# Kernel optimization log

Hardware: AMD Instinct MI355X
Metric: run time of the kernel (lower is better)

Reference implementation:

```python
import jax, jax.numpy as jnp
import numpy as np

B, H, W, C = 16, 64, 64, 512
NH, HD = 16, 32
WH = WW = 8
SHIFT = 4
N = WH * WW
NWIN = (H // WH) * (W // WW)
EPS = 1e-6


def _rel_coords_table():
    rh = np.arange(-(WH - 1), WH, dtype=np.float32)
    rw = np.arange(-(WW - 1), WW, dtype=np.float32)
    t = np.expand_dims(np.transpose(np.stack(np.meshgrid(rh, rw)), (1, 2, 0)), 0)
    t[:, :, :, 0] /= WH - 1
    t[:, :, :, 1] /= WW - 1
    t *= 8
    t = np.sign(t) * np.log2(np.abs(t) + 1.0) / np.log2(8)
    return jnp.asarray(t, jnp.float32)  # (1, 2*WW-1, 2*WH-1, 2)


def _rel_pos_index():
    gx, gy = np.meshgrid(np.arange(WH), np.arange(WW))
    coords = np.stack([gy, gx]).reshape(2, -1)
    rel = (coords[:, :, None] - coords[:, None, :]).transpose(1, 2, 0)
    rel[:, :, 0] += WH - 1
    rel[:, :, 1] += WW - 1
    rel[:, :, 0] *= 2 * WW - 1
    return jnp.asarray(rel.sum(-1).reshape(-1), jnp.int32)  # (N*N,)


def _attn_mask():
    img = np.zeros((H, W), np.float32)
    cnt = 0
    for hs in (slice(0, -WH), slice(-WH, -SHIFT), slice(-SHIFT, None)):
        for ws in (slice(0, -WW), slice(-WW, -SHIFT), slice(-SHIFT, None)):
            img[hs, ws] = cnt
            cnt += 1
    mw = img.reshape(H // WH, WH, W // WW, WW).transpose(0, 2, 1, 3).reshape(-1, N)
    am = mw[:, None, :] - mw[:, :, None]
    return jnp.asarray(np.where(am == 0, 0.0, -100.0), jnp.float32)  # (nW, N, N)


REL_TABLE = _rel_coords_table()
REL_IDX = _rel_pos_index()
ATTN_MASK = _attn_mask()


def _ln(x, g, b):
    m = jnp.mean(x, -1, keepdims=True)
    v = jnp.var(x, -1, keepdims=True)
    return (x - m) * jax.lax.rsqrt(v + EPS) * g + b


def _forward(x, q_w, q_b, k_w, v_w, v_b, proj_w, proj_b, tau,
             cpb_w1, cpb_b1, cpb_w2, cpb_b2,
             norm1_g, norm1_b, norm2_g, norm2_b,
             mlp_w1, mlp_b1, mlp_w2, mlp_b2):
    shortcut = x
    xs = x.reshape(B, H, W, C)
    xs = jnp.roll(xs, shift=(-SHIFT, -SHIFT), axis=(1, 2))  # cyclic shift
    # window partition -> (B*nW, N, C)
    xw = xs.reshape(B, H // WH, WH, W // WW, WW, C).transpose(0, 1, 3, 2, 4, 5).reshape(-1, N, C)
    Bw = B * NWIN
    q = (xw @ q_w + q_b).reshape(Bw, N, NH, HD).transpose(0, 2, 1, 3)
    k = (xw @ k_w).reshape(Bw, N, NH, HD).transpose(0, 2, 1, 3)
    v = (xw @ v_w + v_b).reshape(Bw, N, NH, HD).transpose(0, 2, 1, 3)
    # cosine attention
    qn = jnp.linalg.norm(q, axis=-1)[..., :, None]
    kn = jnp.linalg.norm(k, axis=-1)[..., None, :]
    denom = jnp.maximum(qn * kn, 1e-6)
    attn = jnp.einsum('bhnd,bhmd->bhnm', q, k) / denom
    logit_scale = jnp.maximum(tau + jnp.log(10.0), 0.01)  # (1, NH, 1, 1)
    attn = attn * logit_scale
    # continuous relative position bias MLP
    tbl = jax.nn.relu(REL_TABLE @ cpb_w1 + cpb_b1) @ cpb_w2 + cpb_b2
    tbl = tbl.reshape(-1, NH)
    bias = tbl[REL_IDX].reshape(N, N, NH).transpose(2, 0, 1)
    bias = 16.0 * jax.nn.sigmoid(bias)
    attn = attn + bias[None]
    # shifted-window mask
    attn = attn.reshape(B, NWIN, NH, N, N) + ATTN_MASK[None, :, None]
    attn = jax.nn.softmax(attn.reshape(Bw, NH, N, N), axis=-1)
    out = jnp.einsum('bhnm,bhmd->bhnd', attn, v).transpose(0, 2, 1, 3).reshape(Bw, N, C)
    out = out @ proj_w + proj_b
    # window reverse + reverse shift
    out = out.reshape(B, H // WH, W // WW, WH, WW, C).transpose(0, 1, 3, 2, 4, 5).reshape(B, H, W, C)
    out = jnp.roll(out, shift=(SHIFT, SHIFT), axis=(1, 2)).reshape(B, H * W, C)
    # Swin-V2 post-norm residuals
    x = shortcut + _ln(out, norm1_g, norm1_b)
    h = jax.nn.gelu(x @ mlp_w1 + mlp_b1) @ mlp_w2 + mlp_b2
    x = x + _ln(h, norm2_g, norm2_b)
    return x


def setup_inputs() -> dict:
    key = jax.random.key(0)
    ks = jax.random.split(key, 10)
    s = 0.02
    return {
        'x': jax.random.normal(ks[0], (B, H * W, C), jnp.float32),
        'q_w': jax.random.normal(ks[1], (C, C), jnp.float32) * s,
        'q_b': jnp.zeros((C,), jnp.float32),
        'k_w': jax.random.normal(ks[2], (C, C), jnp.float32) * s,
        'v_w': jax.random.normal(ks[3], (C, C), jnp.float32) * s,
        'v_b': jnp.zeros((C,), jnp.float32),
        'proj_w': jax.random.normal(ks[4], (C, C), jnp.float32) * s,
        'proj_b': jnp.zeros((C,), jnp.float32),
        'tau': jax.random.normal(ks[5], (1, NH, 1, 1), jnp.float32) * s,
        'cpb_w1': jax.random.normal(ks[6], (2, 512), jnp.float32) * s,
        'cpb_b1': jnp.zeros((512,), jnp.float32),
        'cpb_w2': jax.random.normal(ks[7], (512, NH), jnp.float32) * s,
        'cpb_b2': jnp.zeros((NH,), jnp.float32),
        'norm1_g': jnp.ones((C,), jnp.float32),
        'norm1_b': jnp.zeros((C,), jnp.float32),
        'norm2_g': jnp.ones((C,), jnp.float32),
        'norm2_b': jnp.zeros((C,), jnp.float32),
        'mlp_w1': jax.random.normal(ks[8], (C, 4 * C), jnp.float32) * s,
        'mlp_b1': jnp.zeros((4 * C,), jnp.float32),
        'mlp_w2': jax.random.normal(ks[9], (4 * C, C), jnp.float32) * s,
        'mlp_b2': jnp.zeros((C,), jnp.float32),
    }


def reference(x, q_w, q_b, k_w, v_w, v_b, proj_w, proj_b, tau,
              cpb_w1, cpb_b1, cpb_w2, cpb_b2,
              norm1_g, norm1_b, norm2_g, norm2_b,
              mlp_w1, mlp_b1, mlp_w2, mlp_b2):
    return _forward(x, q_w, q_b, k_w, v_w, v_b, proj_w, proj_b, tau,
                    cpb_w1, cpb_b1, cpb_w2, cpb_b2,
                    norm1_g, norm1_b, norm2_g, norm2_b,
                    mlp_w1, mlp_b1, mlp_w2, mlp_b2)
```

## Files before the change

kernel.cpp:

```cpp
#include <hip/hip_runtime.h>
#include <cstdint>
#include <cstddef>

typedef __bf16 bf16x8 __attribute__((ext_vector_type(8)));
typedef float  f32x4  __attribute__((ext_vector_type(4)));
typedef unsigned short u16x8 __attribute__((ext_vector_type(8)));

__device__ __forceinline__ float bf2f(unsigned short u) {
  union { unsigned int u; float f; } v; v.u = ((unsigned int)u) << 16; return v.f;
}
__device__ __forceinline__ unsigned short f2bf(float f) {
  union { float f; unsigned int u; } v; v.f = f;
  return (unsigned short)((v.u + 0x7fffu + ((v.u >> 16) & 1u)) >> 16);
}
__device__ __forceinline__ bf16x8 as_bf(u16x8 u) {
  union { u16x8 a; bf16x8 b; } v; v.a = u; return v.b;
}
__device__ __forceinline__ void g2lds16(const void* g, void* l) {
  __builtin_amdgcn_global_load_lds((__attribute__((address_space(1))) void*)g,
                                   (__attribute__((address_space(3))) void*)l,
                                   16, 0, 0);
}

template<int EPI>
__global__ __launch_bounds__(512, 2) void gemm256(
    const unsigned short* __restrict__ A, const unsigned short* __restrict__ BT,
    const float* __restrict__ bias, unsigned short* __restrict__ C,
    int N, int K, int nbx, int T)
{
  __shared__ __align__(16) unsigned short lds[2][2][2][128 * 64];
  const int tid = threadIdx.x;
  const int wave = tid >> 6, lane = tid & 63;
  const int lm = lane & 15, quad = lane >> 4;
  const int wm2 = wave >> 2, wn4 = wave & 3;
  const int ex = (lm & 7) << 3;

  const int NT = K >> 6;
  const int cpx = T >> 3;
  const int nit = T >> 8;

  const int sl8 = lane >> 3;
  const int scol = ((lane & 7) ^ sl8) << 3;
  const int r0 = wave * 8 + sl8;
  const int aro = r0;
  const int bro = (r0 >> 5) * 64 + (r0 & 31);

  auto stA = [&](const unsigned short* Ab, int bf, int sh, int koff) {
    const unsigned short* s = Ab + (size_t)(sh * 64) * K + koff;
    g2lds16(s,                   &lds[bf][0][sh][wave * 512]);
    g2lds16(s + (size_t)128 * K, &lds[bf][0][sh][4096 + wave * 512]);
  };
  auto stB = [&](const unsigned short* Bb, int bf, int sh, int koff) {
    const unsigned short* s = Bb + (size_t)(sh * 32) * K + koff;
    g2lds16(s,                   &lds[bf][1][sh][wave * 512]);
    g2lds16(s + (size_t)128 * K, &lds[bf][1][sh][4096 + wave * 512]);
  };

  int v = blockIdx.x;
  int wg = (v & 7) * cpx + (v >> 3);
  int bm = wg / nbx, bn = wg % nbx;
  const unsigned short* curA = A + (size_t)(bm * 256 + aro) * K + scol;
  const unsigned short* curB = BT + (size_t)(bn * 256 + bro) * K + scol;

  f32x4 acc[8][4];
  bf16x8 a[4][2], b0[2][2], b1[2][2];

  stA(curA, 0, 0, 0); stB(curB, 0, 0, 0);
  stB(curB, 0, 1, 0); stA(curA, 0, 1, 0);
  stA(curA, 1, 0, 64); stB(curB, 1, 0, 64);
  asm volatile("s_waitcnt vmcnt(4)" ::: "memory");
  __builtin_amdgcn_s_barrier();

  for (int it = 0; it < nit; ++it) {
    int vN = v + 256;
    int wgN = (it + 1 < nit) ? ((vN & 7) * cpx + (vN >> 3)) : wg;
    int bmN = wgN / nbx, bnN = wgN % nbx;
    const unsigned short* nxtA = A + (size_t)(bmN * 256 + aro) * K + scol;
    const unsigned short* nxtB = BT + (size_t)(bnN * 256 + bro) * K + scol;

#pragma unroll
    for (int i = 0; i < 8; i++)
#pragma unroll
      for (int j = 0; j < 4; j++) acc[i][j] = {0.f, 0.f, 0.f, 0.f};

    for (int t = 0; t < NT; ++t) {
      const int b = t & 1;
      const unsigned short *A1, *B1, *A2, *B2; int k1, k2;
      if (t + 1 < NT) { A1 = curA; B1 = curB; k1 = (t + 1) << 6; }
      else            { A1 = nxtA; B1 = nxtB; k1 = 0; }
      if (t + 2 < NT) { A2 = curA; B2 = curB; k2 = (t + 2) << 6; }
      else            { A2 = nxtA; B2 = nxtB; k2 = (t + 2 - NT) << 6; }

#pragma unroll
      for (int mi = 0; mi < 4; mi++)
#pragma unroll
        for (int ks = 0; ks < 2; ks++)
          a[mi][ks] = *(const bf16x8*)&lds[b][0][0][(wm2 * 64 + mi * 16 + lm) * 64 + ((ks * 32 + quad * 8) ^ ex)];
#pragma unroll
      for (int ni = 0; ni < 2; ni++)
#pragma unroll
        for (int ks = 0; ks < 2; ks++)
          b0[ni][ks] = *(const bf16x8*)&lds[b][1][0][(wn4 * 32 + ni * 16 + lm) * 64 + ((ks * 32 + quad * 8) ^ ex)];
      stB(B1, b ^ 1, 1, k1);
      stA(A1, b ^ 1, 1, k1);

      __builtin_amdgcn_s_setprio(1);
#pragma unroll
      for (int ks = 0; ks < 2; ks++)
#pragma unroll
        for (int mi = 0; mi < 4; mi++)
#pragma unroll
          for (int ni = 0; ni < 2; ni++)
            acc[mi][ni] = __builtin_amdgcn_mfma_f32_16x16x32_bf16(a[mi][ks], b0[ni][ks], acc[mi][ni], 0, 0, 0);
      __builtin_amdgcn_s_setprio(0);

#pragma unroll
      for (int ni = 0; ni < 2; ni++)
#pragma unroll
        for (int ks = 0; ks < 2; ks++)
          b1[ni][ks] = *(const bf16x8*)&lds[b][1][1][(wn4 * 32 + ni * 16 + lm) * 64 + ((ks * 32 + quad * 8) ^ ex)];

      __builtin_amdgcn_s_setprio(1);
#pragma unroll
      for (int ks = 0; ks < 2; ks++)
#pragma unroll
        for (int mi = 0; mi < 4; mi++)
#pragma unroll
          for (int ni = 0; ni < 2; ni++)
            acc[mi][2 + ni] = __builtin_amdgcn_mfma_f32_16x16x32_bf16(a[mi][ks], b1[ni][ks], acc[mi][2 + ni], 0, 0, 0);
      __builtin_amdgcn_s_setprio(0);

#pragma unroll
      for (int mi = 0; mi < 4; mi++)
#pragma unroll
        for (int ks = 0; ks < 2; ks++)
          a[mi][ks] = *(const bf16x8*)&lds[b][0][1][(wm2 * 64 + mi * 16 + lm) * 64 + ((ks * 32 + quad * 8) ^ ex)];

      __builtin_amdgcn_s_setprio(1);
#pragma unroll
      for (int ks = 0; ks < 2; ks++)
#pragma unroll
        for (int mi = 0; mi < 4; mi++)
#pragma unroll
          for (int ni = 0; ni < 2; ni++)
            acc[4 + mi][ni] = __builtin_amdgcn_mfma_f32_16x16x32_bf16(a[mi][ks], b0[ni][ks], acc[4 + mi][ni], 0, 0, 0);
      __builtin_amdgcn_s_setprio(0);

      __builtin_amdgcn_s_barrier();

      stA(A2, b, 0, k2);
      stB(B2, b, 0, k2);

      __builtin_amdgcn_s_setprio(1);
#pragma unroll
      for (int ks = 0; ks < 2; ks++)
#pragma unroll
        for (int mi = 0; mi < 4; mi++)
#pragma unroll
          for (int ni = 0; ni < 2; ni++)
            acc[4 + mi][2 + ni] = __builtin_amdgcn_mfma_f32_16x16x32_bf16(a[mi][ks], b1[ni][ks], acc[4 + mi][2 + ni], 0, 0, 0);
      __builtin_amdgcn_s_setprio(0);

      asm volatile("s_waitcnt vmcnt(4)" ::: "memory");
      __builtin_amdgcn_s_barrier();
    }

    float bv[4];
#pragma unroll
    for (int jn = 0; jn < 4; jn++)
      bv[jn] = bias ? bias[bn * 256 + wn4 * 64 + jn * 16 + lm] : 0.f;
    const int rb = bm * 256 + wm2 * 128 + quad * 4;
    const int cb = bn * 256 + wn4 * 64 + lm;
#pragma unroll
    for (int im = 0; im < 8; im++)
#pragma unroll
      for (int jn = 0; jn < 4; jn++)
#pragma unroll
        for (int r = 0; r < 4; r++) {
          float vvv = acc[im][jn][r] + bv[jn];
          if (EPI == 1) {
            float xx = vvv;
            float x2 = xx * xx;
            float tg = xx * fmaf(x2, 0.044715f, 1.0f);
            float e = exp2f(-2.3022083f * tg);
            vvv = xx * __builtin_amdgcn_rcpf(1.f + e);
          }
          C[(size_t)(rb + im * 16 + r) * N + cb + jn * 16] = f2bf(vvv);
        }

    v = vN; wg = wgN; bm = bmN; bn = bnN; curA = nxtA; curB = nxtB;
  }
  asm volatile("s_waitcnt vmcnt(0)" ::: "memory");
}

__global__ __launch_bounds__(256) void transpose_cast(
    const float* __restrict__ W, unsigned short* __restrict__ WT, int K, int N)
{
  __shared__ float t[32][33];
  int bx = blockIdx.x, by = blockIdx.y;
  int tx = threadIdx.x & 31, ty = threadIdx.x >> 5;
#pragma unroll
  for (int j = 0; j < 4; j++)
    t[ty + j * 8][tx] = W[(size_t)(by * 32 + ty + j * 8) * N + bx * 32 + tx];
  __syncthreads();
#pragma unroll
  for (int j = 0; j < 4; j++)
    WT[(size_t)(bx * 32 + ty + j * 8) * K + by * 32 + tx] = f2bf(t[tx][ty + j * 8]);
}

__global__ __launch_bounds__(256) void shift_part(
    const float* __restrict__ x, unsigned short* __restrict__ xw)
{
  int t = blockIdx.x * 256 + threadIdx.x;
  int row = t >> 7;
  int c = (t & 127) * 4;
  int b = row >> 12, rw_ = row & 4095;
  int wi = rw_ >> 6, p = rw_ & 63;
  int hh = (((wi >> 3) * 8 + (p >> 3)) + 4) & 63;
  int ww = (((wi & 7) * 8 + (p & 7)) + 4) & 63;
  const float4 v = *(const float4*)&x[(((size_t)b * 4096) + hh * 64 + ww) * 512 + c];
  ushort4 o;
  o.x = f2bf(v.x); o.y = f2bf(v.y); o.z = f2bf(v.z); o.w = f2bf(v.w);
  *(ushort4*)&xw[(size_t)row * 512 + c] = o;
}

__global__ __launch_bounds__(256) void qkv_bias_kernel(
    const float* __restrict__ qb, const float* __restrict__ vb, float* __restrict__ o)
{
  int t = blockIdx.x * 256 + threadIdx.x;
  float v = 0.f;
  if (t < 512) v = qb[t];
  else if (t >= 1024) v = vb[t - 1024];
  o[t] = v;
}

__device__ __forceinline__ float relsc(int v) {
  float a = fabsf((float)v) * (8.0f / 7.0f);
  float r = log2f(a + 1.f) * (1.f / 3.f);
  return v < 0 ? -r : r;
}
__global__ __launch_bounds__(512) void cpb_kernel(
    const float* __restrict__ w1, const float* __restrict__ b1,
    const float* __restrict__ w2, const float* __restrict__ b2, float* __restrict__ tblT)
{
  __shared__ float hid[512];
  int p = blockIdx.x;
  int i = p / 15, j = p % 15;
  float fr = relsc(i - 7);
  float fc = relsc(j - 7);
  int t = threadIdx.x;
  float hv = fc * w1[t] + fr * w1[512 + t] + b1[t];
  hid[t] = fmaxf(hv, 0.f);
  __syncthreads();
  if (t < 16) {
    float s = b2[t];
    for (int u = 0; u < 512; u++) s += hid[u] * w2[u * 16 + t];
    tblT[t * 225 + p] = 16.f / (1.f + __expf(-s));
  }
}

__global__ __launch_bounds__(256) void attn_mfma(
    const unsigned short* __restrict__ QKV, const float* __restrict__ tau,
    const float* __restrict__ tblT, unsigned short* __restrict__ Om)
{
  __shared__ __align__(16) unsigned short Qs[64 * 32];
  __shared__ __align__(16) unsigned short Ks[64 * 32];
  __shared__ __align__(16) unsigned short Vs[64 * 32];
  __shared__ __align__(16) unsigned short VT[32 * 72];
  __shared__ __align__(16) unsigned short Pb[64 * 72];
  __shared__ float tblh[2][228];
  __shared__ int scode[64];

  const int tid = threadIdx.x;
  const int wave = tid >> 6, lane = tid & 63;
  const int lm = lane & 15, quad = lane >> 4;
  const int w = blockIdx.x >> 1;
  const int hbase = (blockIdx.x & 1) * 8;
  const int wi = w & 63, wr = wi >> 3, wc = wi & 7;
  const size_t wbase = (size_t)w * 64 * 1536;
  const size_t obase = (size_t)w * 64 * 512;

  if (tid < 64) {
    int p = tid;
    int rp = wr * 8 + (p >> 3), cp = wc * 8 + (p & 7);
    scode[p] = (rp < 56 ? 0 : (rp < 60 ? 1 : 2)) * 3 + (cp < 56 ? 0 : (cp < 60 ? 1 : 2));
  }

  const int srow = wave * 16 + (lane >> 2);
  const int scol = (lane & 3) * 8;
  unsigned short* qdst = &Qs[wave * 16 * 32];
  unsigned short* kdst = &Ks[wave * 16 * 32];
  unsigned short* vdst = &Vs[wave * 16 * 32];
  const size_t gs0 = wbase + (size_t)srow * 1536 + scol;

  {
    const size_t g = gs0 + (size_t)hbase * 32;
    g2lds16(QKV + g, qdst);
    g2lds16(QKV + g + 512, kdst);
    g2lds16(QKV + g + 1024, vdst);
    for (int e = tid; e < 225; e += 256) tblh[0][e] = tblT[hbase * 225 + e];
  }

  for (int hh = 0; hh < 8; hh++) {
    const int h = hbase + hh, cur = hh & 1;
    __syncthreads();

    u16x8 au = *(const u16x8*)&Qs[(wave * 16 + lm) * 32 + quad * 8];
    float qss = 0.f;
#pragma unroll
    for (int j = 0; j < 8; j++) { float f = bf2f(au[j]); qss += f * f; }
    qss += __shfl_xor(qss, 16, 64);
    qss += __shfl_xor(qss, 32, 64);
    const float qnv = sqrtf(qss);

    u16x8 bu[4]; float knv[4];
#pragma unroll
    for (int ni = 0; ni < 4; ni++) {
      bu[ni] = *(const u16x8*)&Ks[(ni * 16 + lm) * 32 + quad * 8];
      float kss = 0.f;
#pragma unroll
      for (int j = 0; j < 8; j++) { float f = bf2f(bu[ni][j]); kss += f * f; }
      kss += __shfl_xor(kss, 16, 64);
      kss += __shfl_xor(kss, 32, 64);
      knv[ni] = sqrtf(kss);
    }

    bf16x8 af = as_bf(au);
    f32x4 accS[4];
#pragma unroll
    for (int ni = 0; ni < 4; ni++) {
      f32x4 z = {0.f, 0.f, 0.f, 0.f};
      accS[ni] = __builtin_amdgcn_mfma_f32_16x16x32_bf16(af, as_bf(bu[ni]), z, 0, 0, 0);
    }

    for (int e = tid; e < 2048; e += 256) {
      int d = e & 31, q = e >> 5;
      VT[d * 72 + q] = Vs[q * 32 + d];
    }

    const float scale = fmaxf(tau[h] + 2.302585092994046f, 0.01f);
#pragma unroll
    for (int r = 0; r < 4; r++) {
      int p = wave * 16 + quad * 4 + r;
      float qnp = __shfl(qnv, quad * 4 + r, 64);
      int cp = scode[p];
      float sv[4];
#pragma unroll
      for (int ni = 0; ni < 4; ni++) {
        int q = ni * 16 + lm;
        float denom = fmaxf(qnp * knv[ni], 1e-6f);
        int dr = (p >> 3) - (q >> 3) + 7, dc = (p & 7) - (q & 7) + 7;
        float bv = tblh[cur][dr * 15 + dc];
        float mask = (cp == scode[q]) ? 0.f : -100.f;
        sv[ni] = accS[ni][r] * scale * __builtin_amdgcn_rcpf(denom) + bv + mask;
      }
      float m = fmaxf(fmaxf(sv[0], sv[1]), fmaxf(sv[2], sv[3]));
#pragma unroll
      for (int off = 1; off < 16; off <<= 1) m = fmaxf(m, __shfl_xor(m, off, 64));
      float s = 0.f;
#pragma unroll
      for (int ni = 0; ni < 4; ni++) { sv[ni] = __expf(sv[ni] - m); s += sv[ni]; }
#pragma unroll
      for (int off = 1; off < 16; off <<= 1) s += __shfl_xor(s, off, 64);
      float inv = __builtin_amdgcn_rcpf(s);
#pragma unroll
      for (int ni = 0; ni < 4; ni++)
        Pb[p * 72 + ni * 16 + lm] = f2bf(sv[ni] * inv);
    }

    __syncthreads();

    if (hh < 7) {
      const size_t g = gs0 + (size_t)(h + 1) * 32;
      g2lds16(QKV + g, qdst);
      g2lds16(QKV + g + 512, kdst);
      g2lds16(QKV + g + 1024, vdst);
      for (int e = tid; e < 225; e += 256) tblh[cur ^ 1][e] = tblT[(h + 1) * 225 + e];
    }

    bf16x8 paf[2];
#pragma unroll
    for (int kc = 0; kc < 2; kc++)
      paf[kc] = *reinterpret_cast<const bf16x8*>(&Pb[(wave * 16 + lm) * 72 + kc * 32 + quad * 8]);
    f32x4 accO[2];
#pragma unroll
    for (int n2 = 0; n2 < 2; n2++) {
      f32x4 z = {0.f, 0.f, 0.f, 0.f};
#pragma unroll
      for (int kc = 0; kc < 2; kc++) {
        bf16x8 vb = *reinterpret_cast<const bf16x8*>(&VT[(n2 * 16 + lm) * 72 + kc * 32 + quad * 8]);
        z = __builtin_amdgcn_mfma_f32_16x16x32_bf16(paf[kc], vb, z, 0, 0, 0);
      }
      accO[n2] = z;
    }
#pragma unroll
    for (int n2 = 0; n2 < 2; n2++)
#pragma unroll
      for (int r = 0; r < 4; r++) {
        int p = wave * 16 + quad * 4 + r;
        Om[obase + (size_t)p * 512 + h * 32 + n2 * 16 + lm] = f2bf(accO[n2][r]);
      }
  }
}

__global__ __launch_bounds__(256) void ln1_kernel(
    const float* __restrict__ x, const unsigned short* __restrict__ proj,
    const float* __restrict__ g, const float* __restrict__ b,
    unsigned short* __restrict__ x1b)
{
  int tkn = blockIdx.x * 4 + (threadIdx.x >> 6);
  int lane = threadIdx.x & 63;
  int bb = tkn >> 12, s = tkn & 4095;
  int h_ = s >> 6, w_ = s & 63;
  int r = (h_ + 60) & 63, cc = (w_ + 60) & 63;
  int wi = (r >> 3) * 8 + (cc >> 3);
  int p = (r & 7) * 8 + (cc & 7);
  size_t src = ((size_t)bb * 4096 + wi * 64 + p) * 512 + lane * 8;
  u16x8 pv = *(const u16x8*)&proj[src];
  float v[8]; float ls = 0.f, lq = 0.f;
#pragma unroll
  for (int j = 0; j < 8; j++) { v[j] = bf2f(pv[j]); ls += v[j]; lq += v[j] * v[j]; }
#pragma unroll
  for (int off = 1; off < 64; off <<= 1) {
    ls += __shfl_xor(ls, off, 64);
    lq += __shfl_xor(lq, off, 64);
  }
  float mean = ls * (1.f / 512.f);
  float rstd = rsqrtf(lq * (1.f / 512.f) - mean * mean + 1e-6f);
  int c = lane * 8;
  size_t o = (size_t)tkn * 512 + c;
  float4 xa = *(const float4*)&x[o], xb = *(const float4*)&x[o + 4];
  float4 ga = *(const float4*)&g[c], gb = *(const float4*)&g[c + 4];
  float4 ba = *(const float4*)&b[c], bb4 = *(const float4*)&b[c + 4];
  u16x8 ov;
  ov[0] = f2bf((v[0] - mean) * rstd * ga.x + ba.x + xa.x);
  ov[1] = f2bf((v[1] - mean) * rstd * ga.y + ba.y + xa.y);
  ov[2] = f2bf((v[2] - mean) * rstd * ga.z + ba.z + xa.z);
  ov[3] = f2bf((v[3] - mean) * rstd * ga.w + ba.w + xa.w);
  ov[4] = f2bf((v[4] - mean) * rstd * gb.x + bb4.x + xb.x);
  ov[5] = f2bf((v[5] - mean) * rstd * gb.y + bb4.y + xb.y);
  ov[6] = f2bf((v[6] - mean) * rstd * gb.z + bb4.z + xb.z);
  ov[7] = f2bf((v[7] - mean) * rstd * gb.w + bb4.w + xb.w);
  *(u16x8*)&x1b[o] = ov;
}

__global__ __launch_bounds__(256) void ln2_kernel(
    const unsigned short* __restrict__ x1b, const unsigned short* __restrict__ h2,
    const float* __restrict__ g, const float* __restrict__ b,
    float* __restrict__ out)
{
  int tkn = blockIdx.x * 4 + (threadIdx.x >> 6);
  int lane = threadIdx.x & 63;
  int c = lane * 8;
  size_t o = (size_t)tkn * 512 + c;
  u16x8 hv = *(const u16x8*)&h2[o];
  float v[8]; float ls = 0.f, lq = 0.f;
#pragma unroll
  for (int j = 0; j < 8; j++) { v[j] = bf2f(hv[j]); ls += v[j]; lq += v[j] * v[j]; }
#pragma unroll
  for (int off = 1; off < 64; off <<= 1) {
    ls += __shfl_xor(ls, off, 64);
    lq += __shfl_xor(lq, off, 64);
  }
  float mean = ls * (1.f / 512.f);
  float rstd = rsqrtf(lq * (1.f / 512.f) - mean * mean + 1e-6f);
  u16x8 xv = *(const u16x8*)&x1b[o];
  float4 ga = *(const float4*)&g[c], gb = *(const float4*)&g[c + 4];
  float4 ba = *(const float4*)&b[c], bb4 = *(const float4*)&b[c + 4];
  float4 oa, ob;
  oa.x = bf2f(xv[0]) + (v[0] - mean) * rstd * ga.x + ba.x;
  oa.y = bf2f(xv[1]) + (v[1] - mean) * rstd * ga.y + ba.y;
  oa.z = bf2f(xv[2]) + (v[2] - mean) * rstd * ga.z + ba.z;
  oa.w = bf2f(xv[3]) + (v[3] - mean) * rstd * ga.w + ba.w;
  ob.x = bf2f(xv[4]) + (v[4] - mean) * rstd * gb.x + bb4.x;
  ob.y = bf2f(xv[5]) + (v[5] - mean) * rstd * gb.y + bb4.y;
  ob.z = bf2f(xv[6]) + (v[6] - mean) * rstd * gb.z + bb4.z;
  ob.w = bf2f(xv[7]) + (v[7] - mean) * rstd * gb.w + bb4.w;
  *(float4*)&out[o] = oa;
  *(float4*)&out[o + 4] = ob;
}

extern "C" void kernel_launch(void* const* d_in, const int* in_sizes, int n_in,
                              void* d_out, int out_size, void* d_ws, size_t ws_size,
                              hipStream_t stream) {
  const float* x      = (const float*)d_in[0];
  const float* q_w    = (const float*)d_in[1];
  const float* q_b    = (const float*)d_in[2];
  const float* k_w    = (const float*)d_in[3];
  const float* v_w    = (const float*)d_in[4];
  const float* v_b    = (const float*)d_in[5];
  const float* proj_w = (const float*)d_in[6];
  const float* proj_b = (const float*)d_in[7];
  const float* tau    = (const float*)d_in[8];
  const float* cpb_w1 = (const float*)d_in[9];
  const float* cpb_b1 = (const float*)d_in[10];
  const float* cpb_w2 = (const float*)d_in[11];
  const float* cpb_b2 = (const float*)d_in[12];
  const float* n1g    = (const float*)d_in[13];
  const float* n1b    = (const float*)d_in[14];
  const float* n2g    = (const float*)d_in[15];
  const float* n2b    = (const float*)d_in[16];
  const float* mlp_w1 = (const float*)d_in[17];
  const float* mlp_b1 = (const float*)d_in[18];
  const float* mlp_w2 = (const float*)d_in[19];
  const float* mlp_b2 = (const float*)d_in[20];
  float* out = (float*)d_out;
  char* ws = (char*)d_ws;

  const size_t MB = 1048576;
  unsigned short* xw    = (unsigned short*)(ws + 0 * MB);
  unsigned short* Obuf  = (unsigned short*)(ws + 0 * MB);
  unsigned short* hbuf  = (unsigned short*)(ws + 0 * MB);
  unsigned short* qkv   = (unsigned short*)(ws + 64 * MB);
  unsigned short* projb = (unsigned short*)(ws + 64 * MB);
  unsigned short* x1b   = (unsigned short*)(ws + 128 * MB);
  unsigned short* h2b   = (unsigned short*)(ws + 192 * MB);
  unsigned short* qkvT = (unsigned short*)(ws + 320 * MB);
  unsigned short* pwT  = (unsigned short*)(ws + 320 * MB + 1572864);
  unsigned short* m1T  = (unsigned short*)(ws + 320 * MB + 2097152);
  unsigned short* m2T  = (unsigned short*)(ws + 320 * MB + 4194304);
  float* tbl           = (float*)         (ws + 320 * MB + 6291456);
  float* qkv_b         = (float*)         (ws + 320 * MB + 6307840);

  transpose_cast<<<dim3(16, 16), 256, 0, stream>>>(q_w,    qkvT,          512, 512);
  transpose_cast<<<dim3(16, 16), 256, 0, stream>>>(k_w,    qkvT + 262144, 512, 512);
  transpose_cast<<<dim3(16, 16), 256, 0, stream>>>(v_w,    qkvT + 524288, 512, 512);
  transpose_cast<<<dim3(16, 16), 256, 0, stream>>>(proj_w, pwT, 512, 512);
  transpose_cast<<<dim3(64, 16), 256, 0, stream>>>(mlp_w1, m1T, 512, 2048);
  transpose_cast<<<dim3(16, 64), 256, 0, stream>>>(mlp_w2, m2T, 2048, 512);
  qkv_bias_kernel<<<6, 256, 0, stream>>>(q_b, v_b, qkv_b);
  cpb_kernel<<<225, 512, 0, stream>>>(cpb_w1, cpb_b1, cpb_w2, cpb_b2, tbl);
  shift_part<<<32768, 256, 0, stream>>>(x, xw);
  gemm256<0><<<256, 512, 0, stream>>>(xw, qkvT, qkv_b, qkv, 1536, 512, 6, 1536);
  attn_mfma<<<2048, 256, 0, stream>>>(qkv, tau, tbl, Obuf);
  gemm256<0><<<256, 512, 0, stream>>>(Obuf, pwT, proj_b, projb, 512, 512, 2, 512);
  ln1_kernel<<<16384, 256, 0, stream>>>(x, projb, n1g, n1b, x1b);
  for (int c2 = 0; c2 < 2; c2++) {
    const unsigned short* a = x1b + (size_t)c2 * 32768 * 512;
    unsigned short* h2p = h2b + (size_t)c2 * 32768 * 512;
    gemm256<1><<<256, 512, 0, stream>>>(a, m1T, mlp_b1, hbuf, 2048, 512, 8, 1024);
    gemm256<0><<<256, 512, 0, stream>>>(hbuf, m2T, mlp_b2, h2p, 512, 2048, 2, 256);
  }
  ln2_kernel<<<16384, 256, 0, stream>>>(x1b, h2b, n2g, n2b, out);
}
```

Before: 901.5 us.

## Restructure GEMM main loop into barrier-separated phases with interleaved loads

Reworks the bf16 GEMM inner loop into a four-phase schedule. Each quarter of MFMAs is now fenced by sched_barrier and s_barrier plus an explicit lgkmcnt wait, and the global-to-LDS stores for A and B are spread one per phase. The A fragments are double-buffered in registers (a0/a1), so the second half's A tile can load while earlier MFMAs use the first. This aims for a ping-pong style overlap of LDS reads, global loads and MFMA across waves, at the cost of more workgroup barriers and higher register pressure.

```diff
diff --git a/kernel.cpp b/kernel.cpp
--- a/kernel.cpp
+++ b/kernel.cpp
@@ -63,7 +63,7 @@
   const unsigned short* curB = BT + (size_t)(bn * 256 + bro) * K + scol;
 
   f32x4 acc[8][4];
-  bf16x8 a[4][2], b0[2][2], b1[2][2];
+  bf16x8 a0[4][2], a1[4][2], b0[2][2], b1[2][2];
 
   stA(curA, 0, 0, 0); stB(curB, 0, 0, 0);
   stB(curB, 0, 1, 0); stA(curA, 0, 1, 0);
@@ -85,25 +85,27 @@
 
     for (int t = 0; t < NT; ++t) {
       const int b = t & 1;
-      const unsigned short *A1, *B1, *A2, *B2; int k1, k2;
-      if (t + 1 < NT) { A1 = curA; B1 = curB; k1 = (t + 1) << 6; }
-      else            { A1 = nxtA; B1 = nxtB; k1 = 0; }
-      if (t + 2 < NT) { A2 = curA; B2 = curB; k2 = (t + 2) << 6; }
-      else            { A2 = nxtA; B2 = nxtB; k2 = (t + 2 - NT) << 6; }
+      const unsigned short *A1p, *B1p, *A2p, *B2p; int k1, k2;
+      if (t + 1 < NT) { A1p = curA; B1p = curB; k1 = (t + 1) << 6; }
+      else            { A1p = nxtA; B1p = nxtB; k1 = 0; }
+      if (t + 2 < NT) { A2p = curA; B2p = curB; k2 = (t + 2) << 6; }
+      else            { A2p = nxtA; B2p = nxtB; k2 = (t + 2 - NT) << 6; }
 
 #pragma unroll
       for (int mi = 0; mi < 4; mi++)
 #pragma unroll
         for (int ks = 0; ks < 2; ks++)
-          a[mi][ks] = *(const bf16x8*)&lds[b][0][0][(wm2 * 64 + mi * 16 + lm) * 64 + ((ks * 32 + quad * 8) ^ ex)];
+          a0[mi][ks] = *(const bf16x8*)&lds[b][0][0][(wm2 * 64 + mi * 16 + lm) * 64 + ((ks * 32 + quad * 8) ^ ex)];
 #pragma unroll
       for (int ni = 0; ni < 2; ni++)
 #pragma unroll
         for (int ks = 0; ks < 2; ks++)
           b0[ni][ks] = *(const bf16x8*)&lds[b][1][0][(wn4 * 32 + ni * 16 + lm) * 64 + ((ks * 32 + quad * 8) ^ ex)];
-      stB(B1, b ^ 1, 1, k1);
-      stA(A1, b ^ 1, 1, k1);
-
+      stB(B1p, b ^ 1, 1, k1);
+      __builtin_amdgcn_sched_barrier(0);
+      __builtin_amdgcn_s_barrier();
+      asm volatile("s_waitcnt lgkmcnt(0)" ::: "memory");
+      __builtin_amdgcn_sched_barrier(0);
       __builtin_amdgcn_s_setprio(1);
 #pragma unroll
       for (int ks = 0; ks < 2; ks++)
@@ -111,15 +113,21 @@
         for (int mi = 0; mi < 4; mi++)
 #pragma unroll
           for (int ni = 0; ni < 2; ni++)
-            acc[mi][ni] = __builtin_amdgcn_mfma_f32_16x16x32_bf16(a[mi][ks], b0[ni][ks], acc[mi][ni], 0, 0, 0);
+            acc[mi][ni] = __builtin_amdgcn_mfma_f32_16x16x32_bf16(a0[mi][ks], b0[ni][ks], acc[mi][ni], 0, 0, 0);
       __builtin_amdgcn_s_setprio(0);
+      __builtin_amdgcn_sched_barrier(0);
+      __builtin_amdgcn_s_barrier();
 
 #pragma unroll
       for (int ni = 0; ni < 2; ni++)
 #pragma unroll
         for (int ks = 0; ks < 2; ks++)
           b1[ni][ks] = *(const bf16x8*)&lds[b][1][1][(wn4 * 32 + ni * 16 + lm) * 64 + ((ks * 32 + quad * 8) ^ ex)];
-
+      stA(A1p, b ^ 1, 1, k1);
+      __builtin_amdgcn_sched_barrier(0);
+      __builtin_amdgcn_s_barrier();
+      asm volatile("s_waitcnt lgkmcnt(0)" ::: "memory");
+      __builtin_amdgcn_sched_barrier(0);
       __builtin_amdgcn_s_setprio(1);
 #pragma unroll
       for (int ks = 0; ks < 2; ks++)
@@ -127,15 +135,21 @@
         for (int mi = 0; mi < 4; mi++)
 #pragma unroll
           for (int ni = 0; ni < 2; ni++)
-            acc[mi][2 + ni] = __builtin_amdgcn_mfma_f32_16x16x32_bf16(a[mi][ks], b1[ni][ks], acc[mi][2 + ni], 0, 0, 0);
+            acc[mi][2 + ni] = __builtin_amdgcn_mfma_f32_16x16x32_bf16(a0[mi][ks], b1[ni][ks], acc[mi][2 + ni], 0, 0, 0);
       __builtin_amdgcn_s_setprio(0);
+      __builtin_amdgcn_sched_barrier(0);
+      __builtin_amdgcn_s_barrier();
 
 #pragma unroll
       for (int mi = 0; mi < 4; mi++)
 #pragma unroll
         for (int ks = 0; ks < 2; ks++)
-          a[mi][ks] = *(const bf16x8*)&lds[b][0][1][(wm2 * 64 + mi * 16 + lm) * 64 + ((ks * 32 + quad * 8) ^ ex)];
-
+          a1[mi][ks] = *(const bf16x8*)&lds[b][0][1][(wm2 * 64 + mi * 16 + lm) * 64 + ((ks * 32 + quad * 8) ^ ex)];
+      stA(A2p, b, 0, k2);
+      __builtin_amdgcn_sched_barrier(0);
+      __builtin_amdgcn_s_barrier();
+      asm volatile("s_waitcnt lgkmcnt(0)" ::: "memory");
+      __builtin_amdgcn_sched_barrier(0);
       __builtin_amdgcn_s_setprio(1);
 #pragma unroll
       for (int ks = 0; ks < 2; ks++)
@@ -143,14 +157,14 @@
         for (int mi = 0; mi < 4; mi++)
 #pragma unroll
           for (int ni = 0; ni < 2; ni++)
-            acc[4 + mi][ni] = __builtin_amdgcn_mfma_f32_16x16x32_bf16(a[mi][ks], b0[ni][ks], acc[4 + mi][ni], 0, 0, 0);
+            acc[4 + mi][ni] = __builtin_amdgcn_mfma_f32_16x16x32_bf16(a1[mi][ks], b0[ni][ks], acc[4 + mi][ni], 0, 0, 0);
       __builtin_amdgcn_s_setprio(0);
-
-      __builtin_amdgcn_s_barrier();
-
-      stA(A2, b, 0, k2);
-      stB(B2, b, 0, k2);
-
+      __builtin_amdgcn_sched_barrier(0);
+      __builtin_amdgcn_s_barrier();
+
+      stB(B2p, b, 0, k2);
+      __builtin_amdgcn_sched_barrier(0);
+      __builtin_amdgcn_s_barrier();
       __builtin_amdgcn_s_setprio(1);
 #pragma unroll
       for (int ks = 0; ks < 2; ks++)
@@ -158,9 +172,9 @@
         for (int mi = 0; mi < 4; mi++)
 #pragma unroll
           for (int ni = 0; ni < 2; ni++)
-            acc[4 + mi][2 + ni] = __builtin_amdgcn_mfma_f32_16x16x32_bf16(a[mi][ks], b1[ni][ks], acc[4 + mi][2 + ni], 0, 0, 0);
+            acc[4 + mi][2 + ni] = __builtin_amdgcn_mfma_f32_16x16x32_bf16(a1[mi][ks], b1[ni][ks], acc[4 + mi][2 + ni], 0, 0, 0);
       __builtin_amdgcn_s_setprio(0);
-
+      __builtin_amdgcn_sched_barrier(0);
       asm volatile("s_waitcnt vmcnt(4)" ::: "memory");
       __builtin_amdgcn_s_barrier();
     }
```

New measurement: 916.4 us. Within noise of the previous version (+1.7%).

## Double-buffer A fragments in GEMM k-loop and split attention per head

Applied to the files above, without the earlier changes.

The GEMM main loop is unrolled by two k-steps with hard-coded LDS buffer indices, and the second A-fragment set gets its own registers (a0/a1), which removes per-iteration branch selection and the register reuse hazard. The attention kernel now launches one block per (window, head) instead of looping over 8 heads per block with prefetch, raising parallelism from 2048 to 16384 blocks. The trade-off is higher register pressure in the GEMM and the loss of the intra-block prefetch overlap in attention, plus more block launch overhead.

```diff
diff --git a/kernel.cpp b/kernel.cpp
--- a/kernel.cpp
+++ b/kernel.cpp
@@ -63,7 +63,83 @@
   const unsigned short* curB = BT + (size_t)(bn * 256 + bro) * K + scol;
 
   f32x4 acc[8][4];
-  bf16x8 a[4][2], b0[2][2], b1[2][2];
+  bf16x8 a0[4][2], a1[4][2], b0[2][2], b1[2][2];
+
+  auto kstep = [&](int b, const unsigned short* sA1, const unsigned short* sB1, int k1,
+                   const unsigned short* sA2, const unsigned short* sB2, int k2) {
+#pragma unroll
+    for (int mi = 0; mi < 4; mi++)
+#pragma unroll
+      for (int ks = 0; ks < 2; ks++)
+        a0[mi][ks] = *(const bf16x8*)&lds[b][0][0][(wm2 * 64 + mi * 16 + lm) * 64 + ((ks * 32 + quad * 8) ^ ex)];
+#pragma unroll
+    for (int ni = 0; ni < 2; ni++)
+#pragma unroll
+      for (int ks = 0; ks < 2; ks++)
+        b0[ni][ks] = *(const bf16x8*)&lds[b][1][0][(wn4 * 32 + ni * 16 + lm) * 64 + ((ks * 32 + quad * 8) ^ ex)];
+    stB(sB1, b ^ 1, 1, k1);
+    stA(sA1, b ^ 1, 1, k1);
+
+    __builtin_amdgcn_s_setprio(1);
+#pragma unroll
+    for (int ks = 0; ks < 2; ks++)
+#pragma unroll
+      for (int mi = 0; mi < 4; mi++)
+#pragma unroll
+        for (int ni = 0; ni < 2; ni++)
+          acc[mi][ni] = __builtin_amdgcn_mfma_f32_16x16x32_bf16(a0[mi][ks], b0[ni][ks], acc[mi][ni], 0, 0, 0);
+    __builtin_amdgcn_s_setprio(0);
+
+#pragma unroll
+    for (int ni = 0; ni < 2; ni++)
+#pragma unroll
+      for (int ks = 0; ks < 2; ks++)
+        b1[ni][ks] = *(const bf16x8*)&lds[b][1][1][(wn4 * 32 + ni * 16 + lm) * 64 + ((ks * 32 + quad * 8) ^ ex)];
+
+    __builtin_amdgcn_s_setprio(1);
+#pragma unroll
+    for (int ks = 0; ks < 2; ks++)
+#pragma unroll
+      for (int mi = 0; mi < 4; mi++)
+#pragma unroll
+        for (int ni = 0; ni < 2; ni++)
+          acc[mi][2 + ni] = __builtin_amdgcn_mfma_f32_16x16x32_bf16(a0[mi][ks], b1[ni][ks], acc[mi][2 + ni], 0, 0, 0);
+    __builtin_amdgcn_s_setprio(0);
+
+#pragma unroll
+    for (int mi = 0; mi < 4; mi++)
+#pragma unroll
+      for (int ks = 0; ks < 2; ks++)
+        a1[mi][ks] = *(const bf16x8*)&lds[b][0][1][(wm2 * 64 + mi * 16 + lm) * 64 + ((ks * 32 + quad * 8) ^ ex)];
+
+    __builtin_amdgcn_s_setprio(1);
+#pragma unroll
+    for (int ks = 0; ks < 2; ks++)
+#pragma unroll
+      for (int mi = 0; mi < 4; mi++)
+#pragma unroll
+        for (int ni = 0; ni < 2; ni++)
+          acc[4 + mi][ni] = __builtin_amdgcn_mfma_f32_16x16x32_bf16(a1[mi][ks], b0[ni][ks], acc[4 + mi][ni], 0, 0, 0);
+    __builtin_amdgcn_s_setprio(0);
+
+    __builtin_amdgcn_s_barrier();
+
+    stA(sA2, b, 0, k2);
+    stB(sB2, b, 0, k2);
+
+    __builtin_amdgcn_s_setprio(1);
+#pragma unroll
+    for (int ks = 0; ks < 2; ks++)
+#pragma unroll
+      for (int mi = 0; mi < 4; mi++)
+#pragma unroll
+        for (int ni = 0; ni < 2; ni++)
+          acc[4 + mi][2 + ni] = __builtin_amdgcn_mfma_f32_16x16x32_bf16(a1[mi][ks], b1[ni][ks], acc[4 + mi][2 + ni], 0, 0, 0);
+    __builtin_amdgcn_s_setprio(0);
+
+    asm volatile("s_waitcnt vmcnt(4)" ::: "memory");
+    __builtin_amdgcn_s_barrier();
+  };
 
   stA(curA, 0, 0, 0); stB(curB, 0, 0, 0);
   stB(curB, 0, 1, 0); stA(curA, 0, 1, 0);
@@ -83,87 +159,13 @@
 #pragma unroll
       for (int j = 0; j < 4; j++) acc[i][j] = {0.f, 0.f, 0.f, 0.f};
 
-    for (int t = 0; t < NT; ++t) {
-      const int b = t & 1;
-      const unsigned short *A1, *B1, *A2, *B2; int k1, k2;
-      if (t + 1 < NT) { A1 = curA; B1 = curB; k1 = (t + 1) << 6; }
-      else            { A1 = nxtA; B1 = nxtB; k1 = 0; }
-      if (t + 2 < NT) { A2 = curA; B2 = curB; k2 = (t + 2) << 6; }
-      else            { A2 = nxtA; B2 = nxtB; k2 = (t + 2 - NT) << 6; }
-
-#pragma unroll
-      for (int mi = 0; mi < 4; mi++)
-#pragma unroll
-        for (int ks = 0; ks < 2; ks++)
-          a[mi][ks] = *(const bf16x8*)&lds[b][0][0][(wm2 * 64 + mi * 16 + lm) * 64 + ((ks * 32 + quad * 8) ^ ex)];
-#pragma unroll
-      for (int ni = 0; ni < 2; ni++)
-#pragma unroll
-        for (int ks = 0; ks < 2; ks++)
-          b0[ni][ks] = *(const bf16x8*)&lds[b][1][0][(wn4 * 32 + ni * 16 + lm) * 64 + ((ks * 32 + quad * 8) ^ ex)];
-      stB(B1, b ^ 1, 1, k1);
-      stA(A1, b ^ 1, 1, k1);
-
-      __builtin_amdgcn_s_setprio(1);
-#pragma unroll
-      for (int ks = 0; ks < 2; ks++)
-#pragma unroll
-        for (int mi = 0; mi < 4; mi++)
-#pragma unroll
-          for (int ni = 0; ni < 2; ni++)
-            acc[mi][ni] = __builtin_amdgcn_mfma_f32_16x16x32_bf16(a[mi][ks], b0[ni][ks], acc[mi][ni], 0, 0, 0);
-      __builtin_amdgcn_s_setprio(0);
-
-#pragma unroll
-      for (int ni = 0; ni < 2; ni++)
-#pragma unroll
-        for (int ks = 0; ks < 2; ks++)
-          b1[ni][ks] = *(const bf16x8*)&lds[b][1][1][(wn4 * 32 + ni * 16 + lm) * 64 + ((ks * 32 + quad * 8) ^ ex)];
-
-      __builtin_amdgcn_s_setprio(1);
-#pragma unroll
-      for (int ks = 0; ks < 2; ks++)
-#pragma unroll
-        for (int mi = 0; mi < 4; mi++)
-#pragma unroll
-          for (int ni = 0; ni < 2; ni++)
-            acc[mi][2 + ni] = __builtin_amdgcn_mfma_f32_16x16x32_bf16(a[mi][ks], b1[ni][ks], acc[mi][2 + ni], 0, 0, 0);
-      __builtin_amdgcn_s_setprio(0);
-
-#pragma unroll
-      for (int mi = 0; mi < 4; mi++)
-#pragma unroll
-        for (int ks = 0; ks < 2; ks++)
-          a[mi][ks] = *(const bf16x8*)&lds[b][0][1][(wm2 * 64 + mi * 16 + lm) * 64 + ((ks * 32 + quad * 8) ^ ex)];
-
-      __builtin_amdgcn_s_setprio(1);
-#pragma unroll
-      for (int ks = 0; ks < 2; ks++)
-#pragma unroll
-        for (int mi = 0; mi < 4; mi++)
-#pragma unroll
-          for (int ni = 0; ni < 2; ni++)
-            acc[4 + mi][ni] = __builtin_amdgcn_mfma_f32_16x16x32_bf16(a[mi][ks], b0[ni][ks], acc[4 + mi][ni], 0, 0, 0);
-      __builtin_amdgcn_s_setprio(0);
-
-      __builtin_amdgcn_s_barrier();
-
-      stA(A2, b, 0, k2);
-      stB(B2, b, 0, k2);
-
-      __builtin_amdgcn_s_setprio(1);
-#pragma unroll
-      for (int ks = 0; ks < 2; ks++)
-#pragma unroll
-        for (int mi = 0; mi < 4; mi++)
-#pragma unroll
-          for (int ni = 0; ni < 2; ni++)
-            acc[4 + mi][2 + ni] = __builtin_amdgcn_mfma_f32_16x16x32_bf16(a[mi][ks], b1[ni][ks], acc[4 + mi][2 + ni], 0, 0, 0);
-      __builtin_amdgcn_s_setprio(0);
-
-      asm volatile("s_waitcnt vmcnt(4)" ::: "memory");
-      __builtin_amdgcn_s_barrier();
+#pragma unroll 1
+    for (int t = 0; t < NT - 2; t += 2) {
+      kstep(0, curA, curB, (t + 1) << 6, curA, curB, (t + 2) << 6);
+      kstep(1, curA, curB, (t + 2) << 6, curA, curB, (t + 3) << 6);
     }
+    kstep(0, curA, curB, (NT - 1) << 6, nxtA, nxtB, 0);
+    kstep(1, nxtA, nxtB, 0, nxtA, nxtB, 64);
 
     float bv[4];
 #pragma unroll
@@ -268,14 +270,14 @@
   __shared__ __align__(16) unsigned short Vs[64 * 32];
   __shared__ __align__(16) unsigned short VT[32 * 72];
   __shared__ __align__(16) unsigned short Pb[64 * 72];
-  __shared__ float tblh[2][228];
+  __shared__ float tblh[228];
   __shared__ int scode[64];
 
   const int tid = threadIdx.x;
   const int wave = tid >> 6, lane = tid & 63;
   const int lm = lane & 15, quad = lane >> 4;
-  const int w = blockIdx.x >> 1;
-  const int hbase = (blockIdx.x & 1) * 8;
+  const int w = blockIdx.x >> 4;
+  const int h = blockIdx.x & 15;
   const int wi = w & 63, wr = wi >> 3, wc = wi & 7;
   const size_t wbase = (size_t)w * 64 * 1536;
   const size_t obase = (size_t)w * 64 * 512;
@@ -288,119 +290,102 @@
 
   const int srow = wave * 16 + (lane >> 2);
   const int scol = (lane & 3) * 8;
-  unsigned short* qdst = &Qs[wave * 16 * 32];
-  unsigned short* kdst = &Ks[wave * 16 * 32];
-  unsigned short* vdst = &Vs[wave * 16 * 32];
-  const size_t gs0 = wbase + (size_t)srow * 1536 + scol;
-
   {
-    const size_t g = gs0 + (size_t)hbase * 32;
-    g2lds16(QKV + g, qdst);
-    g2lds16(QKV + g + 512, kdst);
-    g2lds16(QKV + g + 1024, vdst);
-    for (int e = tid; e < 225; e += 256) tblh[0][e] = tblT[hbase * 225 + e];
-  }
-
-  for (int hh = 0; hh < 8; hh++) {
-    const int h = hbase + hh, cur = hh & 1;
-    __syncthreads();
-
-    u16x8 au = *(const u16x8*)&Qs[(wave * 16 + lm) * 32 + quad * 8];
-    float qss = 0.f;
-#pragma unroll
-    for (int j = 0; j < 8; j++) { float f = bf2f(au[j]); qss += f * f; }
-    qss += __shfl_xor(qss, 16, 64);
-    qss += __shfl_xor(qss, 32, 64);
-    const float qnv = sqrtf(qss);
-
-    u16x8 bu[4]; float knv[4];
+    const size_t g = wbase + (size_t)srow * 1536 + (size_t)h * 32 + scol;
+    g2lds16(QKV + g,        &Qs[wave * 16 * 32]);
+    g2lds16(QKV + g + 512,  &Ks[wave * 16 * 32]);
+    g2lds16(QKV + g + 1024, &Vs[wave * 16 * 32]);
+  }
+  for (int e = tid; e < 225; e += 256) tblh[e] = tblT[h * 225 + e];
+  __syncthreads();
+
+  u16x8 au = *(const u16x8*)&Qs[(wave * 16 + lm) * 32 + quad * 8];
+  float qss = 0.f;
+#pragma unroll
+  for (int j = 0; j < 8; j++) { float f = bf2f(au[j]); qss += f * f; }
+  qss += __shfl_xor(qss, 16, 64);
+  qss += __shfl_xor(qss, 32, 64);
+  const float qnv = sqrtf(qss);
+
+  u16x8 bu[4]; float knv[4];
+#pragma unroll
+  for (int ni = 0; ni < 4; ni++) {
+    bu[ni] = *(const u16x8*)&Ks[(ni * 16 + lm) * 32 + quad * 8];
+    float kss = 0.f;
+#pragma unroll
+    for (int j = 0; j < 8; j++) { float f = bf2f(bu[ni][j]); kss += f * f; }
+    kss += __shfl_xor(kss, 16, 64);
+    kss += __shfl_xor(kss, 32, 64);
+    knv[ni] = sqrtf(kss);
+  }
+
+  bf16x8 af = as_bf(au);
+  f32x4 accS[4];
+#pragma unroll
+  for (int ni = 0; ni < 4; ni++) {
+    f32x4 z = {0.f, 0.f, 0.f, 0.f};
+    accS[ni] = __builtin_amdgcn_mfma_f32_16x16x32_bf16(af, as_bf(bu[ni]), z, 0, 0, 0);
+  }
+
+  for (int e = tid; e < 2048; e += 256) {
+    int d = e & 31, q = e >> 5;
+    VT[d * 72 + q] = Vs[q * 32 + d];
+  }
+
+  const float scale = fmaxf(tau[h] + 2.302585092994046f, 0.01f);
+#pragma unroll
+  for (int r = 0; r < 4; r++) {
+    int p = wave * 16 + quad * 4 + r;
+    float qnp = __shfl(qnv, quad * 4 + r, 64);
+    int cp = scode[p];
+    float sv[4];
 #pragma unroll
     for (int ni = 0; ni < 4; ni++) {
-      bu[ni] = *(const u16x8*)&Ks[(ni * 16 + lm) * 32 + quad * 8];
-      float kss = 0.f;
-#pragma unroll
-      for (int j = 0; j < 8; j++) { float f = bf2f(bu[ni][j]); kss += f * f; }
-      kss += __shfl_xor(kss, 16, 64);
-      kss += __shfl_xor(kss, 32, 64);
-      knv[ni] = sqrtf(kss);
+      int q = ni * 16 + lm;
+      float denom = fmaxf(qnp * knv[ni], 1e-6f);
+      int dr = (p >> 3) - (q >> 3) + 7, dc = (p & 7) - (q & 7) + 7;
+      float bv = tblh[dr * 15 + dc];
+      float mask = (cp == scode[q]) ? 0.f : -100.f;
+      sv[ni] = accS[ni][r] * scale * __builtin_amdgcn_rcpf(denom) + bv + mask;
     }
-
-    bf16x8 af = as_bf(au);
-    f32x4 accS[4];
-#pragma unroll
-    for (int ni = 0; ni < 4; ni++) {
-      f32x4 z = {0.f, 0.f, 0.f, 0.f};
-      accS[ni] = __builtin_amdgcn_mfma_f32_16x16x32_bf16(af, as_bf(bu[ni]), z, 0, 0, 0);
+    float m = fmaxf(fmaxf(sv[0], sv[1]), fmaxf(sv[2], sv[3]));
+#pragma unroll
+    for (int off = 1; off < 16; off <<= 1) m = fmaxf(m, __shfl_xor(m, off, 64));
+    float s = 0.f;
+#pragma unroll
+    for (int ni = 0; ni < 4; ni++) { sv[ni] = __expf(sv[ni] - m); s += sv[ni]; }
+#pragma unroll
+    for (int off = 1; off < 16; off <<= 1) s += __shfl_xor(s, off, 64);
+    float inv = __builtin_amdgcn_rcpf(s);
+#pragma unroll
+    for (int ni = 0; ni < 4; ni++)
+      Pb[p * 72 + ni * 16 + lm] = f2bf(sv[ni] * inv);
+  }
+
+  __syncthreads();
+
+  bf16x8 paf[2];
+#pragma unroll
+  for (int kc = 0; kc < 2; kc++)
+    paf[kc] = *reinterpret_cast<const bf16x8*>(&Pb[(wave * 16 + lm) * 72 + kc * 32 + quad * 8]);
+  f32x4 accO[2];
+#pragma unroll
+  for (int n2 = 0; n2 < 2; n2++) {
+    f32x4 z = {0.f, 0.f, 0.f, 0.f};
+#pragma unroll
+    for (int kc = 0; kc < 2; kc++) {
+      bf16x8 vb = *reinterpret_cast<const bf16x8*>(&VT[(n2 * 16 + lm) * 72 + kc * 32 + quad * 8]);
+      z = __builtin_amdgcn_mfma_f32_16x16x32_bf16(paf[kc], vb, z, 0, 0, 0);
     }
-
-    for (int e = tid; e < 2048; e += 256) {
-      int d = e & 31, q = e >> 5;
-      VT[d * 72 + q] = Vs[q * 32 + d];
-    }
-
-    const float scale = fmaxf(tau[h] + 2.302585092994046f, 0.01f);
+    accO[n2] = z;
+  }
+#pragma unroll
+  for (int n2 = 0; n2 < 2; n2++)
 #pragma unroll
     for (int r = 0; r < 4; r++) {
       int p = wave * 16 + quad * 4 + r;
-      float qnp = __shfl(qnv, quad * 4 + r, 64);
-      int cp = scode[p];
-      float sv[4];
-#pragma unroll
-      for (int ni = 0; ni < 4; ni++) {
-        int q = ni * 16 + lm;
-        float denom = fmaxf(qnp * knv[ni], 1e-6f);
-        int dr = (p >> 3) - (q >> 3) + 7, dc = (p & 7) - (q & 7) + 7;
-        float bv = tblh[cur][dr * 15 + dc];
-        float mask = (cp == scode[q]) ? 0.f : -100.f;
-        sv[ni] = accS[ni][r] * scale * __builtin_amdgcn_rcpf(denom) + bv + mask;
-      }
-      float m = fmaxf(fmaxf(sv[0], sv[1]), fmaxf(sv[2], sv[3]));
-#pragma unroll
-      for (int off = 1; off < 16; off <<= 1) m = fmaxf(m, __shfl_xor(m, off, 64));
-      float s = 0.f;
-#pragma unroll
-      for (int ni = 0; ni < 4; ni++) { sv[ni] = __expf(sv[ni] - m); s += sv[ni]; }
-#pragma unroll
-      for (int off = 1; off < 16; off <<= 1) s += __shfl_xor(s, off, 64);
-      float inv = __builtin_amdgcn_rcpf(s);
-#pragma unroll
-      for (int ni = 0; ni < 4; ni++)
-        Pb[p * 72 + ni * 16 + lm] = f2bf(sv[ni] * inv);
+      Om[obase + (size_t)p * 512 + h * 32 + n2 * 16 + lm] = f2bf(accO[n2][r]);
     }
-
-    __syncthreads();
-
-    if (hh < 7) {
-      const size_t g = gs0 + (size_t)(h + 1) * 32;
-      g2lds16(QKV + g, qdst);
-      g2lds16(QKV + g + 512, kdst);
-      g2lds16(QKV + g + 1024, vdst);
-      for (int e = tid; e < 225; e += 256) tblh[cur ^ 1][e] = tblT[(h + 1) * 225 + e];
-    }
-
-    bf16x8 paf[2];
-#pragma unroll
-    for (int kc = 0; kc < 2; kc++)
-      paf[kc] = *reinterpret_cast<const bf16x8*>(&Pb[(wave * 16 + lm) * 72 + kc * 32 + quad * 8]);
-    f32x4 accO[2];
-#pragma unroll
-    for (int n2 = 0; n2 < 2; n2++) {
-      f32x4 z = {0.f, 0.f, 0.f, 0.f};
-#pragma unroll
-      for (int kc = 0; kc < 2; kc++) {
-        bf16x8 vb = *reinterpret_cast<const bf16x8*>(&VT[(n2 * 16 + lm) * 72 + kc * 32 + quad * 8]);
-        z = __builtin_amdgcn_mfma_f32_16x16x32_bf16(paf[kc], vb, z, 0, 0, 0);
-      }
-      accO[n2] = z;
-    }
-#pragma unroll
-    for (int n2 = 0; n2 < 2; n2++)
-#pragma unroll
-      for (int r = 0; r < 4; r++) {
-        int p = wave * 16 + quad * 4 + r;
-        Om[obase + (size_t)p * 512 + h * 32 + n2 * 16 + lm] = f2bf(accO[n2][r]);
-      }
-  }
 }
 
 __global__ __launch_bounds__(256) void ln1_kernel(
@@ -532,7 +517,7 @@
   cpb_kernel<<<225, 512, 0, stream>>>(cpb_w1, cpb_b1, cpb_w2, cpb_b2, tbl);
   shift_part<<<32768, 256, 0, stream>>>(x, xw);
   gemm256<0><<<256, 512, 0, stream>>>(xw, qkvT, qkv_b, qkv, 1536, 512, 6, 1536);
-  attn_mfma<<<2048, 256, 0, stream>>>(qkv, tau, tbl, Obuf);
+  attn_mfma<<<16384, 256, 0, stream>>>(qkv, tau, tbl, Obuf);
   gemm256<0><<<256, 512, 0, stream>>>(Obuf, pwT, proj_b, projb, 512, 512, 2, 512);
   ln1_kernel<<<16384, 256, 0, stream>>>(x, projb, n1g, n1b, x1b);
   for (int c2 = 0; c2 < 2; c2++) {
```

Result: slower. 1.118 ms (+24.0%).
